# Optimization experiments

Hardware: AMD Instinct MI355X
Metric: run time of the kernel (lower is better)

Reference implementation:

```python
import jax, jax.numpy as jnp
import numpy as np

K_NEIGHBORS = 5
EPS = 1e-12  # torch F.normalize eps


def _l2_normalize(x):
    n = jnp.linalg.norm(x, axis=-1, keepdims=True)
    return x / jnp.maximum(n, EPS)


def setup_inputs() -> dict:
    key = jax.random.key(0)
    k1, k2, k3, k4 = jax.random.split(key, 4)
    B, D = 256, 512
    N, A = 50000, 8
    return {
        "z_flowed": jax.random.normal(k1, (B, D), dtype=jnp.float32),
        "target_attrs": jax.random.randint(k2, (B, A), 0, 3, dtype=jnp.int32),
        "train_embeddings": jax.random.normal(k3, (N, D), dtype=jnp.float32),
        "train_attributes": jax.random.randint(k4, (N, A), 0, 3, dtype=jnp.int32),
    }


def reference(z_flowed, target_attrs, train_embeddings, train_attributes):
    B = z_flowed.shape[0]
    A = target_attrs.shape[1]
    z_norm = _l2_normalize(z_flowed)          # [B, D]
    train_norm = _l2_normalize(train_embeddings)  # [N, D]

    # batched attribute match: [B, N] count of matching attributes
    match_score = (train_attributes[None, :, :] == target_attrs[:, None, :]).sum(-1)
    mask = (match_score >= (A - 1)).astype(z_norm.dtype)  # [B, N]

    # cosine similarities for all samples in one GEMM: [B, N]
    sims = jnp.einsum('nd,bd->bn', train_norm, z_norm)
    masked_sim = sims * mask

    top_k_values, _ = jax.lax.top_k(masked_sim, K_NEIGHBORS)  # [B, K]
    per_sample_loss = (1.0 - top_k_values).mean(-1)           # [B]

    # samples with fewer than k matching neighbors are skipped in the sum
    valid = (mask.sum(-1) >= K_NEIGHBORS).astype(per_sample_loss.dtype)
    return (per_sample_loss * valid).sum() / B
```

## Files before the change

### kernel.cpp

```cpp
#include <hip/hip_runtime.h>
#include <math.h>


constexpr int D = 512;
constexpr int A = 8;
constexpr int K_NEI = 5;
constexpr int SLOTS = 512;
constexpr int CSTRIDE = 16;
constexpr int PAIR_CAP = 65536;
constexpr int LDS_PAIR_CAP = 1024;
constexpr int DOT_BLOCKS = 2048;

__device__ __forceinline__ float wave_reduce_add(float v) {
    #pragma unroll
    for (int m = 1; m < 64; m <<= 1) v += __shfl_xor(v, m, 64);
    return v;
}

__global__ __launch_bounds__(64) void prep_kernel(
    const float* __restrict__ z, const int* __restrict__ tattr,
    float* __restrict__ z_norm, unsigned* __restrict__ tpacked,
    int* __restrict__ counters, int* __restrict__ npairs,
    float* __restrict__ out)
{
    const int b = blockIdx.x;
    const int lane = threadIdx.x;
    const float4* zrow = (const float4*)(z + (size_t)b * D);
    float4 v0 = zrow[lane * 2 + 0];
    float4 v1 = zrow[lane * 2 + 1];
    float ss = v0.x*v0.x + v0.y*v0.y + v0.z*v0.z + v0.w*v0.w
             + v1.x*v1.x + v1.y*v1.y + v1.z*v1.z + v1.w*v1.w;
    ss = wave_reduce_add(ss);
    const float scale = 1.0f / fmaxf(sqrtf(ss), 1e-12f);
    v0.x *= scale; v0.y *= scale; v0.z *= scale; v0.w *= scale;
    v1.x *= scale; v1.y *= scale; v1.z *= scale; v1.w *= scale;
    float4* orow = (float4*)(z_norm + (size_t)b * D);
    orow[lane * 2 + 0] = v0;
    orow[lane * 2 + 1] = v1;
    if (lane == 0) {
        unsigned p = 0;
        #pragma unroll
        for (int a = 0; a < A; a++)
            p |= ((unsigned)tattr[b * A + a] & 0xFu) << (4 * a);
        tpacked[b] = p;
        counters[b * CSTRIDE] = 0;
        if (b == 0) { *npairs = 0; out[0] = 0.0f; }
    }
}

__global__ __launch_bounds__(256) void match_kernel(
    const int* __restrict__ trattr, const unsigned* __restrict__ tpacked,
    unsigned* __restrict__ pairs, int* __restrict__ npairs, int N)
{
    __shared__ unsigned s_tp[256];
    __shared__ unsigned s_pairs[LDS_PAIR_CAP];
    __shared__ int s_cnt, s_base;

    const int tid = threadIdx.x;
    const int n = blockIdx.x * 256 + tid;
    s_tp[tid] = tpacked[tid];
    if (tid == 0) s_cnt = 0;
    __syncthreads();

    if (n < N) {
        const int4* a4 = (const int4*)(trattr + (size_t)n * A);
        const int4 x = a4[0], y = a4[1];
        const unsigned p =
             ((unsigned)x.x & 0xFu)        | (((unsigned)x.y & 0xFu) << 4)
           | (((unsigned)x.z & 0xFu) << 8)  | (((unsigned)x.w & 0xFu) << 12)
           | (((unsigned)y.x & 0xFu) << 16) | (((unsigned)y.y & 0xFu) << 20)
           | (((unsigned)y.z & 0xFu) << 24) | (((unsigned)y.w & 0xFu) << 28);

        const uint4* tp4 = (const uint4*)s_tp;
        #pragma unroll 4
        for (int bq = 0; bq < 64; bq++) {
            const uint4 t = tp4[bq];
            #pragma unroll
            for (int j = 0; j < 4; j++) {
                const unsigned tv = (j == 0) ? t.x : (j == 1) ? t.y : (j == 2) ? t.z : t.w;
                const unsigned yv = p ^ tv;
                const unsigned nzhi = ((((yv & 0x77777777u) + 0x77777777u) | yv) & 0x88888888u);
                if (__popc(nzhi) <= 1) {
                    const int idx = atomicAdd(&s_cnt, 1);
                    if (idx < LDS_PAIR_CAP)
                        s_pairs[idx] = ((unsigned)n << 8) | (unsigned)(bq * 4 + j);
                }
            }
        }
    }
    __syncthreads();
    const int cnt = min(s_cnt, LDS_PAIR_CAP);
    if (tid == 0) s_base = atomicAdd(npairs, cnt);
    __syncthreads();
    const int base = s_base;
    for (int i = tid; i < cnt; i += 256)
        if (base + i < PAIR_CAP) pairs[base + i] = s_pairs[i];
}

__global__ __launch_bounds__(256) void dot_kernel(
    const float* __restrict__ train, const float* __restrict__ z_norm,
    const unsigned* __restrict__ pairs, const int* __restrict__ npairs,
    int* __restrict__ counters, float* __restrict__ simbuf)
{
    const int lane = threadIdx.x & 63;
    const int w = blockIdx.x * 4 + (threadIdx.x >> 6);
    const int nwaves = DOT_BLOCKS * 4;
    const int np = min(*npairs, PAIR_CAP);

    const int niter = (np - w + nwaves - 1) / nwaves;
    if (niter <= 0) return;
    const int myidx = w + lane * nwaves;
    const unsigned mypr = (myidx < np && lane < niter) ? pairs[myidx] : 0u;

    unsigned pr = __shfl(mypr, 0, 64);
    const float4* row4 = (const float4*)(train  + (size_t)(pr >> 8)   * D);
    const float4* zr4  = (const float4*)(z_norm + (size_t)(pr & 255u) * D);
    float4 r0 = row4[lane * 2 + 0];
    float4 r1 = row4[lane * 2 + 1];
    float4 z0 = zr4[lane * 2 + 0];
    float4 z1 = zr4[lane * 2 + 1];

    for (int t = 0; t < niter; t++) {
        float4 nr0, nr1, nz0, nz1;
        const bool more = (t + 1 < niter);
        if (more) {
            const unsigned npr = __shfl(mypr, t + 1, 64);
            const float4* nrow4 = (const float4*)(train  + (size_t)(npr >> 8)   * D);
            const float4* nzr4  = (const float4*)(z_norm + (size_t)(npr & 255u) * D);
            nr0 = nrow4[lane * 2 + 0];
            nr1 = nrow4[lane * 2 + 1];
            nz0 = nzr4[lane * 2 + 0];
            nz1 = nzr4[lane * 2 + 1];
        }

        float ss = r0.x*r0.x + r0.y*r0.y + r0.z*r0.z + r0.w*r0.w
                 + r1.x*r1.x + r1.y*r1.y + r1.z*r1.z + r1.w*r1.w;
        float dd = r0.x*z0.x + r0.y*z0.y + r0.z*z0.z + r0.w*z0.w
                 + r1.x*z1.x + r1.y*z1.y + r1.z*z1.z + r1.w*z1.w;
        #pragma unroll
        for (int m = 1; m < 64; m <<= 1) {
            ss += __shfl_xor(ss, m, 64);
            dd += __shfl_xor(dd, m, 64);
        }
        if (lane == 0) {
            const int b = (int)(pr & 255u);
            const float sim = dd / fmaxf(sqrtf(ss), 1e-12f);
            const int idx = atomicAdd(&counters[b * CSTRIDE], 1);
            if (idx < SLOTS) simbuf[(size_t)b * SLOTS + idx] = sim;
        }

        if (more) {
            pr = __shfl(mypr, t + 1, 64);
            r0 = nr0; r1 = nr1; z0 = nz0; z1 = nz1;
        }
    }
}

__global__ __launch_bounds__(64) void topk_kernel(
    const int* __restrict__ counters, const float* __restrict__ simbuf,
    float* __restrict__ out, int Bt)
{
    const int b = blockIdx.x;
    const int lane = threadIdx.x;
    const int cnt = counters[b * CSTRIDE];
    const int m = min(cnt, SLOTS);
    const float* buf = simbuf + (size_t)b * SLOTS;

    float v[8];
    #pragma unroll
    for (int k = 0; k < 8; k++) {
        const int i = lane + k * 64;
        v[k] = (i < m) ? buf[i] : -1e30f;
    }

    float s = 0.0f;
    #pragma unroll
    for (int r = 0; r < K_NEI; r++) {
        float best = v[0];
        #pragma unroll
        for (int k = 1; k < 8; k++) best = fmaxf(best, v[k]);
        float M = best;
        #pragma unroll
        for (int mm = 1; mm < 64; mm <<= 1) M = fmaxf(M, __shfl_xor(M, mm, 64));
        s += fmaxf(M, 0.0f);
        const unsigned long long bal = __ballot(best == M);
        const int first = __ffsll(bal) - 1;
        if (lane == first) {
            if      (v[0] == M) v[0] = -1e30f;
            else if (v[1] == M) v[1] = -1e30f;
            else if (v[2] == M) v[2] = -1e30f;
            else if (v[3] == M) v[3] = -1e30f;
            else if (v[4] == M) v[4] = -1e30f;
            else if (v[5] == M) v[5] = -1e30f;
            else if (v[6] == M) v[6] = -1e30f;
            else                v[7] = -1e30f;
        }
    }

    if (lane == 0) {
        const float contrib = (cnt >= K_NEI) ? (1.0f - s * (1.0f / K_NEI)) : 0.0f;
        atomicAdd(out, contrib / (float)Bt);
    }
}

extern "C" void kernel_launch(void* const* d_in, const int* in_sizes, int n_in,
                              void* d_out, int out_size, void* d_ws, size_t ws_size,
                              hipStream_t stream)
{
    const float* z      = (const float*)d_in[0];
    const int*   tattr  = (const int*)d_in[1];
    const float* train  = (const float*)d_in[2];
    const int*   trattr = (const int*)d_in[3];
    float* out = (float*)d_out;

    const int B = in_sizes[0] / D;
    const int N = in_sizes[2] / D;

    char* ws = (char*)d_ws;
    float*    z_norm   = (float*)ws;    ws += (size_t)B * D * sizeof(float);
    unsigned* tpacked  = (unsigned*)ws; ws += (size_t)B * sizeof(unsigned);
    int*      counters = (int*)ws;      ws += (size_t)B * CSTRIDE * sizeof(int);
    float*    simbuf   = (float*)ws;    ws += (size_t)B * SLOTS * sizeof(float);
    int*      npairs   = (int*)ws;      ws += 64;
    unsigned* pairs    = (unsigned*)ws;

    prep_kernel<<<B, 64, 0, stream>>>(z, tattr, z_norm, tpacked, counters, npairs, out);
    match_kernel<<<(N + 255) / 256, 256, 0, stream>>>(trattr, tpacked, pairs, npairs, N);
    dot_kernel<<<DOT_BLOCKS, 256, 0, stream>>>(train, z_norm, pairs, npairs, counters, simbuf);
    topk_kernel<<<B, 64, 0, stream>>>(counters, simbuf, out, B);
}
```

Measured before the change: 177.7 us.

## Process each pair with a 16-lane group instead of a full wave in dot kernel

The dot kernel now gives each pair to a 16-lane subgroup, so one wave works on four pairs at once. Each lane loads eight float4s of the train row and of the z row, and the shuffle reduction shrinks to four steps. The explicit register double-buffer prefetch is gone; latency hiding now comes from more pairs in flight per wave. DOT_BLOCKS goes up to cover the new mapping. The cost is more registers per lane and fewer full-wave coalesced loads per row.

```diff
diff --git a/kernel.cpp b/kernel.cpp
--- a/kernel.cpp
+++ b/kernel.cpp
@@ -9,7 +9,7 @@
 constexpr int CSTRIDE = 16;
 constexpr int PAIR_CAP = 65536;
 constexpr int LDS_PAIR_CAP = 1024;
-constexpr int DOT_BLOCKS = 2048;
+constexpr int DOT_BLOCKS = 2304;
 
 __device__ __forceinline__ float wave_reduce_add(float v) {
     #pragma unroll
@@ -102,43 +102,30 @@
     const unsigned* __restrict__ pairs, const int* __restrict__ npairs,
     int* __restrict__ counters, float* __restrict__ simbuf)
 {
-    const int lane = threadIdx.x & 63;
-    const int w = blockIdx.x * 4 + (threadIdx.x >> 6);
-    const int nwaves = DOT_BLOCKS * 4;
+    const int lane = threadIdx.x & 15;
+    const int g0 = blockIdx.x * 16 + (threadIdx.x >> 4);
+    const int ngroups = DOT_BLOCKS * 16;
     const int np = min(*npairs, PAIR_CAP);
 
-    const int niter = (np - w + nwaves - 1) / nwaves;
-    if (niter <= 0) return;
-    const int myidx = w + lane * nwaves;
-    const unsigned mypr = (myidx < np && lane < niter) ? pairs[myidx] : 0u;
-
-    unsigned pr = __shfl(mypr, 0, 64);
-    const float4* row4 = (const float4*)(train  + (size_t)(pr >> 8)   * D);
-    const float4* zr4  = (const float4*)(z_norm + (size_t)(pr & 255u) * D);
-    float4 r0 = row4[lane * 2 + 0];
-    float4 r1 = row4[lane * 2 + 1];
-    float4 z0 = zr4[lane * 2 + 0];
-    float4 z1 = zr4[lane * 2 + 1];
-
-    for (int t = 0; t < niter; t++) {
-        float4 nr0, nr1, nz0, nz1;
-        const bool more = (t + 1 < niter);
-        if (more) {
-            const unsigned npr = __shfl(mypr, t + 1, 64);
-            const float4* nrow4 = (const float4*)(train  + (size_t)(npr >> 8)   * D);
-            const float4* nzr4  = (const float4*)(z_norm + (size_t)(npr & 255u) * D);
-            nr0 = nrow4[lane * 2 + 0];
-            nr1 = nrow4[lane * 2 + 1];
-            nz0 = nzr4[lane * 2 + 0];
-            nz1 = nzr4[lane * 2 + 1];
-        }
-
-        float ss = r0.x*r0.x + r0.y*r0.y + r0.z*r0.z + r0.w*r0.w
-                 + r1.x*r1.x + r1.y*r1.y + r1.z*r1.z + r1.w*r1.w;
-        float dd = r0.x*z0.x + r0.y*z0.y + r0.z*z0.z + r0.w*z0.w
-                 + r1.x*z1.x + r1.y*z1.y + r1.z*z1.z + r1.w*z1.w;
-        #pragma unroll
-        for (int m = 1; m < 64; m <<= 1) {
+    for (int i = g0; i < np; i += ngroups) {
+        const unsigned pr = pairs[i];
+        const float4* __restrict__ row4 = (const float4*)(train  + (size_t)(pr >> 8)   * D);
+        const float4* __restrict__ zr4  = (const float4*)(z_norm + (size_t)(pr & 255u) * D);
+
+        float4 r[8], zz[8];
+        #pragma unroll
+        for (int j = 0; j < 8; j++) r[j]  = row4[j * 16 + lane];
+        #pragma unroll
+        for (int j = 0; j < 8; j++) zz[j] = zr4[j * 16 + lane];
+
+        float ss = 0.0f, dd = 0.0f;
+        #pragma unroll
+        for (int j = 0; j < 8; j++) {
+            ss += r[j].x*r[j].x  + r[j].y*r[j].y  + r[j].z*r[j].z  + r[j].w*r[j].w;
+            dd += r[j].x*zz[j].x + r[j].y*zz[j].y + r[j].z*zz[j].z + r[j].w*zz[j].w;
+        }
+        #pragma unroll
+        for (int m = 1; m < 16; m <<= 1) {
             ss += __shfl_xor(ss, m, 64);
             dd += __shfl_xor(dd, m, 64);
         }
@@ -147,11 +134,6 @@
             const float sim = dd / fmaxf(sqrtf(ss), 1e-12f);
             const int idx = atomicAdd(&counters[b * CSTRIDE], 1);
             if (idx < SLOTS) simbuf[(size_t)b * SLOTS + idx] = sim;
-        }
-
-        if (more) {
-            pr = __shfl(mypr, t + 1, 64);
-            r0 = nr0; r1 = nr1; z0 = nz0; z1 = nz1;
         }
     }
 }
```

After: 176.4 us (median of 2 runs). Within noise of the previous version (-0.7%).
